# Kernel optimization log

Measured on AMD Instinct MI355X. Metric: run time of the kernel, lower is better.

The kernel has to match this reference:

```python
import jax, jax.numpy as jnp
import numpy as np

B, T, S = 1, 8, 1024
HID, H = 1152, 16
D = HID // H  # 72
EPS = 1e-6


def rmsnorm(t, gamma):
    # t: [b,t,s,h,d], gamma: [h,d] per-head learnable scale (QKNorm)
    var = jnp.mean(jnp.square(t), axis=-1, keepdims=True)
    return t * jax.lax.rsqrt(var + EPS) * gamma


def setup_inputs() -> dict:
    key = jax.random.key(0)
    ks = jax.random.split(key, 8)
    sc = lambda fan_in: 1.0 / np.sqrt(fan_in)
    x = jax.random.normal(ks[0], (B, T, S, HID), dtype=jnp.float32)
    Wq = jax.random.normal(ks[1], (HID, HID), dtype=jnp.float32) * sc(HID)
    bq = jnp.zeros((HID,), dtype=jnp.float32)
    Wkv = jax.random.normal(ks[2], (HID, 2 * HID), dtype=jnp.float32) * sc(HID)
    bkv = jnp.zeros((2 * HID,), dtype=jnp.float32)
    q_gamma = jnp.ones((H, D), dtype=jnp.float32)
    k_gamma = jnp.ones((H, D), dtype=jnp.float32)
    Wo = jax.random.normal(ks[3], (HID, HID), dtype=jnp.float32) * sc(HID)
    return {"x": x, "Wq": Wq, "bq": bq, "Wkv": Wkv, "bkv": bkv,
            "q_gamma": q_gamma, "k_gamma": k_gamma, "Wo": Wo}


def reference(x, Wq, bq, Wkv, bkv, q_gamma, k_gamma, Wo):
    b, t, s, _ = x.shape
    q = (x @ Wq + bq).reshape(b, t, s, H, D)
    kv = x @ Wkv + bkv
    k, v = jnp.split(kv, 2, axis=-1)
    k = k.reshape(b, t, s, H, D)
    v = v.reshape(b, t, s, H, D)
    q = rmsnorm(q, q_gamma)
    k = rmsnorm(k, k_gamma)
    # NOTE: original applies no 1/sqrt(d) scaling (QKNorm replaces it)
    attn_weight = jnp.einsum('btqhd,btkhd->bthqk', q, k)
    attn = jax.nn.softmax(attn_weight, axis=-1)
    out = jnp.einsum('bthqk,btkhd->btqhd', attn, v).reshape(b, t, s, HID)
    return out @ Wo
```

## Files before the change

kernel.cpp:

```cpp
#include <hip/hip_runtime.h>


typedef __attribute__((ext_vector_type(4))) short s16x4;
typedef __attribute__((ext_vector_type(8))) short s16x8;
typedef __attribute__((ext_vector_type(4))) float f32x4;
typedef __attribute__((ext_vector_type(16))) float f32x16;
typedef __attribute__((ext_vector_type(4))) int i32x4;

__device__ __forceinline__ unsigned short f2b(float x) {
  unsigned u = __float_as_uint(x);
  u += 0x7FFFu + ((u >> 16) & 1u);
  return (unsigned short)(u >> 16);
}
__device__ __forceinline__ float b2f(unsigned short u) {
  return __uint_as_float(((unsigned)u) << 16);
}
__device__ __forceinline__ void gld16(const void* g, void* l) {
  __builtin_amdgcn_global_load_lds(
      (const __attribute__((address_space(1))) void*)g,
      (__attribute__((address_space(3))) void*)l, 16, 0, 0);
}

__global__ __launch_bounds__(256) void cvt_bf16_kernel(const float* __restrict__ in,
                                                       unsigned short* __restrict__ out,
                                                       int n16) {
  int i = blockIdx.x * 256 + threadIdx.x;
  if (i >= n16) return;
  const float4* p = (const float4*)(in + (size_t)i * 16);
  float4 a = p[0], b = p[1], c = p[2], d = p[3];
  s16x8 r0, r1;
  r0[0] = (short)f2b(a.x); r0[1] = (short)f2b(a.y); r0[2] = (short)f2b(a.z); r0[3] = (short)f2b(a.w);
  r0[4] = (short)f2b(c.x); r0[5] = (short)f2b(c.y); r0[6] = (short)f2b(c.z); r0[7] = (short)f2b(c.w);
  r1[0] = (short)f2b(b.x); r1[1] = (short)f2b(b.y); r1[2] = (short)f2b(b.z); r1[3] = (short)f2b(b.w);
  r1[4] = (short)f2b(d.x); r1[5] = (short)f2b(d.y); r1[6] = (short)f2b(d.z); r1[7] = (short)f2b(d.w);
  *(s16x8*)(out + (size_t)i * 16) = r0;
  *(s16x8*)(out + (size_t)i * 16 + 8) = r1;
}

__global__ __launch_bounds__(256) void transpose_cvt3_kernel(
    const float* __restrict__ Wq, const float* __restrict__ Wkv,
    const float* __restrict__ Wo, unsigned short* __restrict__ WqT,
    unsigned short* __restrict__ WkvT, unsigned short* __restrict__ WoT) {
  constexpr int K = 1152;
  int id = blockIdx.x;
  const float* W;
  unsigned short* WT;
  int N;
  if (id < 1296) { W = Wq; WT = WqT; N = 1152; }
  else if (id < 3888) { W = Wkv; WT = WkvT; N = 2304; id -= 1296; }
  else { W = Wo; WT = WoT; N = 1152; id -= 3888; }
  int ntiles = N / 32;
  int bxx = id % ntiles, byy = id / ntiles;
  __shared__ float tile[32][33];
  int n0 = bxx * 32, k0 = byy * 32;
  int tx = threadIdx.x & 31, ty = threadIdx.x >> 5;
#pragma unroll
  for (int i = 0; i < 4; i++)
    tile[ty + i * 8][tx] = W[(size_t)(k0 + ty + i * 8) * N + n0 + tx];
  __syncthreads();
  int stx = (tx & 19) | ((tx & 4) << 1) | ((tx & 8) >> 1);
#pragma unroll
  for (int i = 0; i < 4; i++)
    WT[(size_t)(n0 + ty + i * 8) * K + k0 + stx] = f2b(tile[tx][ty + i * 8]);
}

__global__ __launch_bounds__(256) void gemm_qkv_kernel(const unsigned short* __restrict__ A,
                                                       const unsigned short* __restrict__ BT,
                                                       const float* __restrict__ biasq,
                                                       const float* __restrict__ biaskv,
                                                       unsigned short* __restrict__ qn,
                                                       unsigned short* __restrict__ kn,
                                                       unsigned short* __restrict__ vt) {
  constexpr int K = 1152;
  constexpr int NT = K / 32;
  __shared__ __align__(16) unsigned short LDSU[3 * 8192 + 3 * 4096];
  unsigned short* As = LDSU;
  unsigned short* Bs = LDSU + 3 * 8192;
  int tid = threadIdx.x;
  int lane = tid & 63, wave = tid >> 6;
  int wr = (wave >> 1) * 128, wc = (wave & 1) * 64;
  int l31 = lane & 31, lh = lane >> 5;
  int bid = blockIdx.x;
  int xcd = bid & 7;
  int w = bid >> 3;
  int st = w / 12, inner = w - st * 12;
  int ibx = inner % 3, iby = inner / 3;
  int bx = st * 3 + ibx;
  int by = xcd * 4 + iby;
  int brow = by * 256, bcol = bx * 128;
  const unsigned short* AsrcP[4];
  const unsigned short* BsrcP[2];
  int dstA[4], dstB[2];
#pragma unroll
  for (int i = 0; i < 4; i++) {
    int c = tid + 256 * i;
    int row = c >> 2, j = c & 3;
    AsrcP[i] = A + (size_t)(brow + row) * K + (j ^ ((row >> 1) & 3)) * 8;
    dstA[i] = (wave * 64 + 256 * i) * 8;
  }
#pragma unroll
  for (int i = 0; i < 2; i++) {
    int c = tid + 256 * i;
    int row = c >> 2, j = c & 3;
    BsrcP[i] = BT + (size_t)(bcol + row) * K + (j ^ ((row >> 1) & 3)) * 8;
    dstB[i] = (wave * 64 + 256 * i) * 8;
  }
#define STAGE(KT, BUF)                                           \
  {                                                              \
    int kb = (KT) * 32;                                          \
    gld16(AsrcP[0] + kb, &As[(BUF) * 8192 + dstA[0]]);           \
    gld16(AsrcP[1] + kb, &As[(BUF) * 8192 + dstA[1]]);           \
    gld16(AsrcP[2] + kb, &As[(BUF) * 8192 + dstA[2]]);           \
    gld16(AsrcP[3] + kb, &As[(BUF) * 8192 + dstA[3]]);           \
    gld16(BsrcP[0] + kb, &Bs[(BUF) * 4096 + dstB[0]]);           \
    gld16(BsrcP[1] + kb, &Bs[(BUF) * 4096 + dstB[1]]);           \
  }
  int fr = (l31 >> 1) & 3;
  int slotk[2] = {(lh ^ fr) * 8, ((2 + lh) ^ fr) * 8};
  STAGE(0, 0);
  STAGE(1, 1);
  f32x16 acc[4][2] = {};
  int cur = 0;
  for (int kt = 0; kt < NT; kt++) {
    if (kt < NT - 1)
      asm volatile("s_waitcnt vmcnt(6)\n\ts_barrier" ::: "memory");
    else
      asm volatile("s_waitcnt vmcnt(0)\n\ts_barrier" ::: "memory");
    if (kt + 2 < NT) {
      int nb = (cur == 0) ? 2 : cur - 1;
      STAGE(kt + 2, nb);
    }
    int ab = cur * 8192, bb = cur * 4096;
#pragma unroll
    for (int kk = 0; kk < 2; kk++) {
      int so = slotk[kk];
      s16x8 af[4], bf[2];
#pragma unroll
      for (int m = 0; m < 4; m++)
        af[m] = *(const s16x8*)&As[ab + (wr + m * 32 + l31) * 32 + so];
#pragma unroll
      for (int n = 0; n < 2; n++)
        bf[n] = *(const s16x8*)&Bs[bb + (wc + n * 32 + l31) * 32 + so];
      __builtin_amdgcn_s_setprio(1);
#pragma unroll
      for (int m = 0; m < 4; m++)
#pragma unroll
        for (int n = 0; n < 2; n++)
          acc[m][n] = __builtin_amdgcn_mfma_f32_32x32x16_bf16(af[m], bf[n], acc[m][n], 0, 0, 0);
      __builtin_amdgcn_s_setprio(0);
    }
    cur = (cur == 2) ? 0 : cur + 1;
  }
#undef STAGE
  if (bcol >= 2304) {
    __syncthreads();
    int c0 = bcol - 2304;
#pragma unroll
    for (int m = 0; m < 4; m++) {
#pragma unroll
      for (int n = 0; n < 2; n++) {
        int col = wc + n * 32 + l31;
        float bias = biaskv[1152 + c0 + col];
#pragma unroll
        for (int reg = 0; reg < 16; reg++) {
          int row = wr + m * 32 + (reg & 3) + 8 * (reg >> 2) + 4 * lh;
          LDSU[col * 264 + row] = f2b(acc[m][n][reg] + bias);
        }
      }
    }
    __syncthreads();
    int t = brow >> 10, sbase = brow & 1023;
#pragma unroll
    for (int i = 0; i < 16; i++) {
      int id = tid + 256 * i;
      int col = id >> 5, rowc = id & 31;
      int c = c0 + col;
      int h = c / 72, d = c - h * 72;
      s16x8 v8 = *(const s16x8*)&LDSU[col * 264 + rowc * 8];
      *(s16x8*)(vt + ((size_t)((t * 16 + h) * 80 + d)) * 1024 + sbase + rowc * 8) = v8;
    }
  } else {
#pragma unroll
    for (int m = 0; m < 4; m++) {
#pragma unroll
      for (int n = 0; n < 2; n++) {
        int gcol = bcol + wc + n * 32 + l31;
        float bias = (gcol < 1152) ? biasq[gcol] : biaskv[gcol - 1152];
        int c = (gcol < 1152) ? gcol : gcol - 1152;
        int h = c / 72, d = c - h * 72;
        unsigned short* dst = (gcol < 1152) ? qn : kn;
#pragma unroll
        for (int reg = 0; reg < 16; reg++) {
          int grow = brow + wr + m * 32 + (reg & 3) + 8 * (reg >> 2) + 4 * lh;
          float v = acc[m][n][reg] + bias;
          int t = grow >> 10, s = grow & 1023;
          dst[((size_t)((t * 16 + h) * 1024 + s)) * 96 + d] = f2b(v);
        }
      }
    }
  }
}

__global__ __launch_bounds__(256) void gemm_out_kernel(const unsigned short* __restrict__ A,
                                                       const unsigned short* __restrict__ BT,
                                                       int N, int gx,
                                                       float* __restrict__ outF) {
  constexpr int K = 1152;
  constexpr int NT = K / 32;
  __shared__ __align__(16) unsigned short As[3 * 4096];
  __shared__ __align__(16) unsigned short Bs[3 * 4096];
  int tid = threadIdx.x;
  int lane = tid & 63, wave = tid >> 6;
  int wr = (wave >> 1) * 64, wc = (wave & 1) * 64;
  int l31 = lane & 31, lh = lane >> 5;
  int bid = blockIdx.x;
  int xcd = bid & 7;
  int w = bid >> 3;
  int st = w / 24, inner = w - st * 24;
  int ibx = inner % 3, iby = inner / 3;
  int bx = st * 3 + ibx;
  int by = xcd * 8 + iby;
  int brow = by * 128, bcol = bx * 128;
  const unsigned short* AsrcP[2];
  const unsigned short* BsrcP[2];
  int dst0[2];
#pragma unroll
  for (int i = 0; i < 2; i++) {
    int c = tid + 256 * i;
    int row = c >> 2, j = c & 3;
    int ch = j ^ ((row >> 1) & 3);
    AsrcP[i] = A + (size_t)(brow + row) * K + ch * 8;
    BsrcP[i] = BT + (size_t)(bcol + row) * K + ch * 8;
    dst0[i] = (wave * 64 + 256 * i) * 8;
  }
#define STAGE(KT, BUF)                                          \
  {                                                             \
    int kb = (KT) * 32;                                         \
    gld16(AsrcP[0] + kb, &As[(BUF) * 4096 + dst0[0]]);          \
    gld16(BsrcP[0] + kb, &Bs[(BUF) * 4096 + dst0[0]]);          \
    gld16(AsrcP[1] + kb, &As[(BUF) * 4096 + dst0[1]]);          \
    gld16(BsrcP[1] + kb, &Bs[(BUF) * 4096 + dst0[1]]);          \
  }
  int fr = (l31 >> 1) & 3;
  int slotk[2] = {(lh ^ fr) * 8, ((2 + lh) ^ fr) * 8};
  STAGE(0, 0);
  STAGE(1, 1);
  f32x16 acc[2][2] = {};
  int cur = 0;
  for (int kt = 0; kt < NT; kt++) {
    if (kt < NT - 1)
      asm volatile("s_waitcnt vmcnt(4)\n\ts_barrier" ::: "memory");
    else
      asm volatile("s_waitcnt vmcnt(0)\n\ts_barrier" ::: "memory");
    if (kt + 2 < NT) {
      int nb = (cur == 0) ? 2 : cur - 1;
      STAGE(kt + 2, nb);
    }
    int ab = cur * 4096;
#pragma unroll
    for (int kk = 0; kk < 2; kk++) {
      int so = slotk[kk];
      s16x8 af[2], bf[2];
#pragma unroll
      for (int m = 0; m < 2; m++)
        af[m] = *(const s16x8*)&As[ab + (wr + m * 32 + l31) * 32 + so];
#pragma unroll
      for (int n = 0; n < 2; n++)
        bf[n] = *(const s16x8*)&Bs[ab + (wc + n * 32 + l31) * 32 + so];
      __builtin_amdgcn_s_setprio(1);
#pragma unroll
      for (int m = 0; m < 2; m++)
#pragma unroll
        for (int n = 0; n < 2; n++)
          acc[m][n] = __builtin_amdgcn_mfma_f32_32x32x16_bf16(af[m], bf[n], acc[m][n], 0, 0, 0);
      __builtin_amdgcn_s_setprio(0);
    }
    cur = (cur == 2) ? 0 : cur + 1;
  }
#undef STAGE
#pragma unroll
  for (int m = 0; m < 2; m++) {
#pragma unroll
    for (int n = 0; n < 2; n++) {
#pragma unroll
      for (int reg = 0; reg < 16; reg++) {
        int grow = brow + wr + m * 32 + (reg & 3) + 8 * (reg >> 2) + 4 * lh;
        int gcol = bcol + wc + n * 32 + l31;
        outF[(size_t)grow * N + gcol] = acc[m][n][reg];
      }
    }
  }
}

__global__ __launch_bounds__(256) void rmsnorm2_kernel(unsigned short* __restrict__ qn,
                                                       unsigned short* __restrict__ kn,
                                                       const float* __restrict__ qg,
                                                       const float* __restrict__ kg) {
  int r = blockIdx.x * 4 + (threadIdx.x >> 6);
  int isK = r >= 131072;
  int g = isK ? r - 131072 : r;
  unsigned short* buf = isK ? kn : qn;
  const float* gamma = isK ? kg : qg;
  int h = (g >> 10) & 15;
  size_t base = (size_t)g * 96;
  int l = threadIdx.x & 63;
  float e0 = b2f(buf[base + l]);
  float e1 = 0.f;
  if (l < 8) e1 = b2f(buf[base + 64 + l]);
  float ss = e0 * e0 + e1 * e1;
#pragma unroll
  for (int m = 1; m < 64; m <<= 1) ss += __shfl_xor(ss, m);
  float sc = rsqrtf(ss * (1.0f / 72.0f) + 1e-6f);
  buf[base + l] = f2b(e0 * sc * gamma[h * 72 + l]);
  if (l < 32) {
    float v = 0.f;
    if (l < 8) v = e1 * sc * gamma[h * 72 + 64 + l];
    buf[base + 64 + l] = f2b(v);
  }
}

__global__ __launch_bounds__(256) void attn_kernel(const unsigned short* __restrict__ Qn,
                                                   const unsigned short* __restrict__ Kn,
                                                   const unsigned short* __restrict__ VtG,
                                                   unsigned short* __restrict__ att) {
  __shared__ unsigned short Kl[2][64][100];
  __shared__ unsigned short Vt[80][76];
  int tid = threadIdx.x;
  int lane = tid & 63, wave = tid >> 6;
  int l15 = lane & 15, lq = lane >> 4, kf = lq * 4;
  int bid = blockIdx.x;
  int orig = (bid & 7) * 128 + (bid >> 3);
  int qb = orig & 7, th = orig >> 3;
  int t = th >> 4, h = th & 15;
  const unsigned short* Q = Qn + (size_t)th * 1024 * 96;
  const unsigned short* Kp = Kn + (size_t)th * 1024 * 96;
  const unsigned short* Vg = VtG + (size_t)th * 80 * 1024;
  int qrow0 = qb * 128 + wave * 32;
  int krow[3], kco[3], vd[3], vco[3];
#pragma unroll
  for (int i = 0; i < 3; i++) {
    int c = tid + i * 256;
    krow[i] = c / 12;
    kco[i] = c - 12 * krow[i];
    int cc = tid + i * 256;
    vd[i] = cc >> 3;
    vco[i] = cc & 7;
  }
  bool v2 = tid < 128;
  s16x8 sk[3], sv[3];
  s16x8 qf0[3], qf1[3];
#pragma unroll
  for (int c = 0; c < 3; c++) {
    const unsigned short* p0 = Q + (size_t)(qrow0 + l15) * 96 + c * 32 + kf;
    s16x4 lo = *(const s16x4*)p0;
    s16x4 hi = *(const s16x4*)(p0 + 16);
    qf0[c] = __builtin_shufflevector(lo, hi, 0, 1, 2, 3, 4, 5, 6, 7);
    const unsigned short* p1 = Q + (size_t)(qrow0 + 16 + l15) * 96 + c * 32 + kf;
    s16x4 lo1 = *(const s16x4*)p1;
    s16x4 hi1 = *(const s16x4*)(p1 + 16);
    qf1[c] = __builtin_shufflevector(lo1, hi1, 0, 1, 2, 3, 4, 5, 6, 7);
  }
  f32x4 o[2][5] = {};
  float m_r[2] = {-3.0e38f, -3.0e38f}, l_r[2] = {0.f, 0.f};

#pragma unroll
  for (int i = 0; i < 3; i++)
    sk[i] = *(const s16x8*)(Kp + (size_t)krow[i] * 96 + kco[i] * 8);
#pragma unroll
  for (int i = 0; i < 2; i++)
    sv[i] = *(const s16x8*)(Vg + (size_t)vd[i] * 1024 + vco[i] * 8);
  if (v2) sv[2] = *(const s16x8*)(Vg + (size_t)vd[2] * 1024 + vco[2] * 8);
#pragma unroll
  for (int i = 0; i < 3; i++) *(s16x8*)&Kl[0][krow[i]][kco[i] * 8] = sk[i];
#pragma unroll
  for (int i = 0; i < 2; i++) *(s16x8*)&Vt[vd[i]][vco[i] * 8] = sv[i];
  if (v2) *(s16x8*)&Vt[vd[2]][vco[2] * 8] = sv[2];

  for (int tt = 0; tt < 16; tt++) {
    __syncthreads();
    int cur = tt & 1;
    if (tt < 15) {
      int kv1 = (tt + 1) * 64;
#pragma unroll
      for (int i = 0; i < 3; i++)
        sk[i] = *(const s16x8*)(Kp + (size_t)(kv1 + krow[i]) * 96 + kco[i] * 8);
#pragma unroll
      for (int i = 0; i < 2; i++)
        sv[i] = *(const s16x8*)(Vg + (size_t)vd[i] * 1024 + kv1 + vco[i] * 8);
      if (v2) sv[2] = *(const s16x8*)(Vg + (size_t)vd[2] * 1024 + kv1 + vco[2] * 8);
    }
    f32x4 st0[4], st1[4];
    __builtin_amdgcn_s_setprio(1);
#pragma unroll
    for (int n = 0; n < 4; n++) {
      f32x4 a0 = {}, a1 = {};
#pragma unroll
      for (int c = 0; c < 3; c++) {
        s16x4 lo = *(const s16x4*)&Kl[cur][n * 16 + l15][c * 32 + kf];
        s16x4 hi = *(const s16x4*)&Kl[cur][n * 16 + l15][c * 32 + kf + 16];
        s16x8 kfr = __builtin_shufflevector(lo, hi, 0, 1, 2, 3, 4, 5, 6, 7);
        a0 = __builtin_amdgcn_mfma_f32_16x16x32_bf16(kfr, qf0[c], a0, 0, 0, 0);
        a1 = __builtin_amdgcn_mfma_f32_16x16x32_bf16(kfr, qf1[c], a1, 0, 0, 0);
      }
      st0[n] = a0;
      st1[n] = a1;
    }
    __builtin_amdgcn_s_setprio(0);
#define SOFTMAX(ST, G)                                                        \
    {                                                                         \
      float tmax = ST[0][0];                                                  \
      _Pragma("unroll") for (int n = 0; n < 4; n++)                           \
        _Pragma("unroll") for (int r = 0; r < 4; r++)                         \
          tmax = fmaxf(tmax, ST[n][r]);                                       \
      tmax = fmaxf(tmax, __shfl_xor(tmax, 16));                               \
      tmax = fmaxf(tmax, __shfl_xor(tmax, 32));                               \
      bool up = !__all(tmax <= m_r[G]);                                       \
      float scale = 1.0f;                                                     \
      if (up) {                                                               \
        float mn = fmaxf(m_r[G], tmax);                                       \
        scale = __expf(m_r[G] - mn);                                          \
        m_r[G] = mn;                                                          \
      }                                                                       \
      float sum = 0.f;                                                        \
      _Pragma("unroll") for (int n = 0; n < 4; n++)                           \
        _Pragma("unroll") for (int r = 0; r < 4; r++) {                       \
          float p = __expf(ST[n][r] - m_r[G]);                                \
          ST[n][r] = p;                                                       \
          sum += p;                                                           \
        }                                                                     \
      sum += __shfl_xor(sum, 16);                                             \
      sum += __shfl_xor(sum, 32);                                             \
      if (up) {                                                               \
        l_r[G] = l_r[G] * scale + sum;                                        \
        _Pragma("unroll") for (int r = 0; r < 4; r++) {                       \
          float scq = __shfl(scale, 4 * lq + r);                              \
          _Pragma("unroll") for (int v = 0; v < 5; v++) o[G][v][r] *= scq;    \
        }                                                                     \
      } else {                                                                \
        l_r[G] += sum;                                                        \
      }                                                                       \
    }
#define PV(ST, G)                                                             \
    {                                                                         \
      __builtin_amdgcn_s_setprio(1);                                          \
      _Pragma("unroll") for (int b = 0; b < 2; b++) {                         \
        int w0, w1, w2, w3;                                                   \
        asm("v_cvt_pk_bf16_f32 %0, %1, %2" : "=v"(w0)                         \
            : "v"(ST[2 * b][0]), "v"(ST[2 * b][1]));                          \
        asm("v_cvt_pk_bf16_f32 %0, %1, %2" : "=v"(w1)                         \
            : "v"(ST[2 * b][2]), "v"(ST[2 * b][3]));                          \
        asm("v_cvt_pk_bf16_f32 %0, %1, %2" : "=v"(w2)                         \
            : "v"(ST[2 * b + 1][0]), "v"(ST[2 * b + 1][1]));                  \
        asm("v_cvt_pk_bf16_f32 %0, %1, %2" : "=v"(w3)                         \
            : "v"(ST[2 * b + 1][2]), "v"(ST[2 * b + 1][3]));                  \
        i32x4 pw = {w0, w1, w2, w3};                                          \
        s16x8 pf = __builtin_bit_cast(s16x8, pw);                             \
        _Pragma("unroll") for (int v = 0; v < 5; v++) {                       \
          s16x4 vlo = *(const s16x4*)&Vt[v * 16 + l15][b * 32 + kf];          \
          s16x4 vhi = *(const s16x4*)&Vt[v * 16 + l15][b * 32 + kf + 16];     \
          s16x8 vf = __builtin_shufflevector(vlo, vhi, 0, 1, 2, 3, 4, 5, 6, 7);\
          o[G][v] = __builtin_amdgcn_mfma_f32_16x16x32_bf16(pf, vf, o[G][v], 0, 0, 0); \
        }                                                                     \
      }                                                                       \
      __builtin_amdgcn_s_setprio(0);                                          \
    }
    SOFTMAX(st0, 0);
    PV(st0, 0);
    SOFTMAX(st1, 1);
    PV(st1, 1);
#undef SOFTMAX
#undef PV
    if (tt < 15) {
      __syncthreads();
      int nxt = cur ^ 1;
#pragma unroll
      for (int i = 0; i < 3; i++) *(s16x8*)&Kl[nxt][krow[i]][kco[i] * 8] = sk[i];
#pragma unroll
      for (int i = 0; i < 2; i++) *(s16x8*)&Vt[vd[i]][vco[i] * 8] = sv[i];
      if (v2) *(s16x8*)&Vt[vd[2]][vco[2] * 8] = sv[2];
    }
  }
#pragma unroll
  for (int g = 0; g < 2; g++)
#pragma unroll
    for (int r = 0; r < 4; r++) {
      float inv = 1.0f / __shfl(l_r[g], 4 * lq + r);
      int qrow = qrow0 + g * 16 + 4 * lq + r;
      size_t rowbase = (size_t)(t * 1024 + qrow) * 1152;
#pragma unroll
      for (int v = 0; v < 5; v++) {
        int d = v * 16 + l15;
        if (d < 72) {
          int col = h * 72 + d;
          int scol = (col & ~12) | ((col & 4) << 1) | ((col & 8) >> 1);
          att[rowbase + scol] = f2b(o[g][v][r] * inv);
        }
      }
    }
}

extern "C" void kernel_launch(void* const* d_in, const int* in_sizes, int n_in,
                              void* d_out, int out_size, void* d_ws, size_t ws_size,
                              hipStream_t stream) {
  const float* x   = (const float*)d_in[0];
  const float* Wq  = (const float*)d_in[1];
  const float* bq  = (const float*)d_in[2];
  const float* Wkv = (const float*)d_in[3];
  const float* bkv = (const float*)d_in[4];
  const float* qg  = (const float*)d_in[5];
  const float* kg  = (const float*)d_in[6];
  const float* Wo  = (const float*)d_in[7];
  float* out = (float*)d_out;

  char* w = (char*)d_ws;
  unsigned short* xb   = (unsigned short*)w; w += (size_t)8192 * 1152 * 2;
  unsigned short* WqT  = (unsigned short*)w; w += (size_t)1152 * 1152 * 2;
  unsigned short* WkvT = (unsigned short*)w; w += (size_t)2304 * 1152 * 2;
  unsigned short* WoT  = (unsigned short*)w; w += (size_t)1152 * 1152 * 2;
  unsigned short* qn   = (unsigned short*)w; w += (size_t)128 * 1024 * 96 * 2;
  unsigned short* kn   = (unsigned short*)w; w += (size_t)128 * 1024 * 96 * 2;
  unsigned short* vt   = (unsigned short*)w; w += (size_t)128 * 80 * 1024 * 2;
  unsigned short* att  = (unsigned short*)w; w += (size_t)8192 * 1152 * 2;

  cvt_bf16_kernel<<<2304, 256, 0, stream>>>(x, xb, 9437184 / 16);
  transpose_cvt3_kernel<<<5184, 256, 0, stream>>>(Wq, Wkv, Wo, WqT, WkvT, WoT);

  gemm_qkv_kernel<<<864, 256, 0, stream>>>(xb, WqT, bq, bkv, qn, kn, vt);
  rmsnorm2_kernel<<<65536, 256, 0, stream>>>(qn, kn, qg, kg);

  attn_kernel<<<1024, 256, 0, stream>>>(qn, kn, vt, att);

  gemm_out_kernel<<<576, 256, 0, stream>>>(att, WoT, 1152, 9, out);
}
```

Before: 302.4 us.

## Enlarge output GEMM tile to 256x128 and share V fragments across query groups

The output projection GEMM now uses 256x128 block tiles, with each wave computing 128x64. This halves the grid to 288 blocks and re-maps block indices per XCD. It raises data reuse per loaded tile, at the cost of more LDS and accumulator registers and fewer blocks than the 256 CUs. In the attention kernel, PV for both query groups now runs after both softmaxes and shares each V fragment load between two MFMAs, which cuts LDS reads but keeps both probability tiles live longer.

```diff
diff --git a/kernel.cpp b/kernel.cpp
--- a/kernel.cpp
+++ b/kernel.cpp
@@ -203,73 +203,77 @@
 
 __global__ __launch_bounds__(256) void gemm_out_kernel(const unsigned short* __restrict__ A,
                                                        const unsigned short* __restrict__ BT,
-                                                       int N, int gx,
                                                        float* __restrict__ outF) {
   constexpr int K = 1152;
   constexpr int NT = K / 32;
-  __shared__ __align__(16) unsigned short As[3 * 4096];
+  __shared__ __align__(16) unsigned short As[3 * 8192];
   __shared__ __align__(16) unsigned short Bs[3 * 4096];
   int tid = threadIdx.x;
   int lane = tid & 63, wave = tid >> 6;
-  int wr = (wave >> 1) * 64, wc = (wave & 1) * 64;
+  int wr = (wave >> 1) * 128, wc = (wave & 1) * 64;
   int l31 = lane & 31, lh = lane >> 5;
   int bid = blockIdx.x;
   int xcd = bid & 7;
   int w = bid >> 3;
-  int st = w / 24, inner = w - st * 24;
-  int ibx = inner % 3, iby = inner / 3;
-  int bx = st * 3 + ibx;
-  int by = xcd * 8 + iby;
-  int brow = by * 128, bcol = bx * 128;
-  const unsigned short* AsrcP[2];
+  int iby = w / 9, bx = w - iby * 9;
+  int by = xcd * 4 + iby;
+  int brow = by * 256, bcol = bx * 128;
+  const unsigned short* AsrcP[4];
   const unsigned short* BsrcP[2];
-  int dst0[2];
+  int dstA[4], dstB[2];
+#pragma unroll
+  for (int i = 0; i < 4; i++) {
+    int c = tid + 256 * i;
+    int row = c >> 2, j = c & 3;
+    AsrcP[i] = A + (size_t)(brow + row) * K + (j ^ ((row >> 1) & 3)) * 8;
+    dstA[i] = (wave * 64 + 256 * i) * 8;
+  }
 #pragma unroll
   for (int i = 0; i < 2; i++) {
     int c = tid + 256 * i;
     int row = c >> 2, j = c & 3;
-    int ch = j ^ ((row >> 1) & 3);
-    AsrcP[i] = A + (size_t)(brow + row) * K + ch * 8;
-    BsrcP[i] = BT + (size_t)(bcol + row) * K + ch * 8;
-    dst0[i] = (wave * 64 + 256 * i) * 8;
-  }
-#define STAGE(KT, BUF)                                          \
-  {                                                             \
-    int kb = (KT) * 32;                                         \
-    gld16(AsrcP[0] + kb, &As[(BUF) * 4096 + dst0[0]]);          \
-    gld16(BsrcP[0] + kb, &Bs[(BUF) * 4096 + dst0[0]]);          \
-    gld16(AsrcP[1] + kb, &As[(BUF) * 4096 + dst0[1]]);          \
-    gld16(BsrcP[1] + kb, &Bs[(BUF) * 4096 + dst0[1]]);          \
+    BsrcP[i] = BT + (size_t)(bcol + row) * K + (j ^ ((row >> 1) & 3)) * 8;
+    dstB[i] = (wave * 64 + 256 * i) * 8;
+  }
+#define STAGE(KT, BUF)                                           \
+  {                                                              \
+    int kb = (KT) * 32;                                          \
+    gld16(AsrcP[0] + kb, &As[(BUF) * 8192 + dstA[0]]);           \
+    gld16(AsrcP[1] + kb, &As[(BUF) * 8192 + dstA[1]]);           \
+    gld16(AsrcP[2] + kb, &As[(BUF) * 8192 + dstA[2]]);           \
+    gld16(AsrcP[3] + kb, &As[(BUF) * 8192 + dstA[3]]);           \
+    gld16(BsrcP[0] + kb, &Bs[(BUF) * 4096 + dstB[0]]);           \
+    gld16(BsrcP[1] + kb, &Bs[(BUF) * 4096 + dstB[1]]);           \
   }
   int fr = (l31 >> 1) & 3;
   int slotk[2] = {(lh ^ fr) * 8, ((2 + lh) ^ fr) * 8};
   STAGE(0, 0);
   STAGE(1, 1);
-  f32x16 acc[2][2] = {};
+  f32x16 acc[4][2] = {};
   int cur = 0;
   for (int kt = 0; kt < NT; kt++) {
     if (kt < NT - 1)
-      asm volatile("s_waitcnt vmcnt(4)\n\ts_barrier" ::: "memory");
+      asm volatile("s_waitcnt vmcnt(6)\n\ts_barrier" ::: "memory");
     else
       asm volatile("s_waitcnt vmcnt(0)\n\ts_barrier" ::: "memory");
     if (kt + 2 < NT) {
       int nb = (cur == 0) ? 2 : cur - 1;
       STAGE(kt + 2, nb);
     }
-    int ab = cur * 4096;
+    int ab = cur * 8192, bb = cur * 4096;
 #pragma unroll
     for (int kk = 0; kk < 2; kk++) {
       int so = slotk[kk];
-      s16x8 af[2], bf[2];
-#pragma unroll
-      for (int m = 0; m < 2; m++)
+      s16x8 af[4], bf[2];
+#pragma unroll
+      for (int m = 0; m < 4; m++)
         af[m] = *(const s16x8*)&As[ab + (wr + m * 32 + l31) * 32 + so];
 #pragma unroll
       for (int n = 0; n < 2; n++)
-        bf[n] = *(const s16x8*)&Bs[ab + (wc + n * 32 + l31) * 32 + so];
+        bf[n] = *(const s16x8*)&Bs[bb + (wc + n * 32 + l31) * 32 + so];
       __builtin_amdgcn_s_setprio(1);
 #pragma unroll
-      for (int m = 0; m < 2; m++)
+      for (int m = 0; m < 4; m++)
 #pragma unroll
         for (int n = 0; n < 2; n++)
           acc[m][n] = __builtin_amdgcn_mfma_f32_32x32x16_bf16(af[m], bf[n], acc[m][n], 0, 0, 0);
@@ -279,14 +283,14 @@
   }
 #undef STAGE
 #pragma unroll
-  for (int m = 0; m < 2; m++) {
+  for (int m = 0; m < 4; m++) {
 #pragma unroll
     for (int n = 0; n < 2; n++) {
 #pragma unroll
       for (int reg = 0; reg < 16; reg++) {
         int grow = brow + wr + m * 32 + (reg & 3) + 8 * (reg >> 2) + 4 * lh;
         int gcol = bcol + wc + n * 32 + l31;
-        outF[(size_t)grow * N + gcol] = acc[m][n][reg];
+        outF[(size_t)grow * 1152 + gcol] = acc[m][n][reg];
       }
     }
   }
@@ -440,36 +444,35 @@
         l_r[G] += sum;                                                        \
       }                                                                       \
     }
-#define PV(ST, G)                                                             \
-    {                                                                         \
-      __builtin_amdgcn_s_setprio(1);                                          \
-      _Pragma("unroll") for (int b = 0; b < 2; b++) {                         \
-        int w0, w1, w2, w3;                                                   \
-        asm("v_cvt_pk_bf16_f32 %0, %1, %2" : "=v"(w0)                         \
-            : "v"(ST[2 * b][0]), "v"(ST[2 * b][1]));                          \
-        asm("v_cvt_pk_bf16_f32 %0, %1, %2" : "=v"(w1)                         \
-            : "v"(ST[2 * b][2]), "v"(ST[2 * b][3]));                          \
-        asm("v_cvt_pk_bf16_f32 %0, %1, %2" : "=v"(w2)                         \
-            : "v"(ST[2 * b + 1][0]), "v"(ST[2 * b + 1][1]));                  \
-        asm("v_cvt_pk_bf16_f32 %0, %1, %2" : "=v"(w3)                         \
-            : "v"(ST[2 * b + 1][2]), "v"(ST[2 * b + 1][3]));                  \
-        i32x4 pw = {w0, w1, w2, w3};                                          \
-        s16x8 pf = __builtin_bit_cast(s16x8, pw);                             \
-        _Pragma("unroll") for (int v = 0; v < 5; v++) {                       \
-          s16x4 vlo = *(const s16x4*)&Vt[v * 16 + l15][b * 32 + kf];          \
-          s16x4 vhi = *(const s16x4*)&Vt[v * 16 + l15][b * 32 + kf + 16];     \
-          s16x8 vf = __builtin_shufflevector(vlo, vhi, 0, 1, 2, 3, 4, 5, 6, 7);\
-          o[G][v] = __builtin_amdgcn_mfma_f32_16x16x32_bf16(pf, vf, o[G][v], 0, 0, 0); \
-        }                                                                     \
-      }                                                                       \
-      __builtin_amdgcn_s_setprio(0);                                          \
-    }
     SOFTMAX(st0, 0);
-    PV(st0, 0);
     SOFTMAX(st1, 1);
-    PV(st1, 1);
 #undef SOFTMAX
-#undef PV
+    __builtin_amdgcn_s_setprio(1);
+#pragma unroll
+    for (int b = 0; b < 2; b++) {
+      int a0, a1, a2, a3, b0w, b1w, b2w, b3w;
+      asm("v_cvt_pk_bf16_f32 %0, %1, %2" : "=v"(a0) : "v"(st0[2 * b][0]), "v"(st0[2 * b][1]));
+      asm("v_cvt_pk_bf16_f32 %0, %1, %2" : "=v"(a1) : "v"(st0[2 * b][2]), "v"(st0[2 * b][3]));
+      asm("v_cvt_pk_bf16_f32 %0, %1, %2" : "=v"(a2) : "v"(st0[2 * b + 1][0]), "v"(st0[2 * b + 1][1]));
+      asm("v_cvt_pk_bf16_f32 %0, %1, %2" : "=v"(a3) : "v"(st0[2 * b + 1][2]), "v"(st0[2 * b + 1][3]));
+      asm("v_cvt_pk_bf16_f32 %0, %1, %2" : "=v"(b0w) : "v"(st1[2 * b][0]), "v"(st1[2 * b][1]));
+      asm("v_cvt_pk_bf16_f32 %0, %1, %2" : "=v"(b1w) : "v"(st1[2 * b][2]), "v"(st1[2 * b][3]));
+      asm("v_cvt_pk_bf16_f32 %0, %1, %2" : "=v"(b2w) : "v"(st1[2 * b + 1][0]), "v"(st1[2 * b + 1][1]));
+      asm("v_cvt_pk_bf16_f32 %0, %1, %2" : "=v"(b3w) : "v"(st1[2 * b + 1][2]), "v"(st1[2 * b + 1][3]));
+      i32x4 pw0 = {a0, a1, a2, a3};
+      i32x4 pw1 = {b0w, b1w, b2w, b3w};
+      s16x8 pf0 = __builtin_bit_cast(s16x8, pw0);
+      s16x8 pf1 = __builtin_bit_cast(s16x8, pw1);
+#pragma unroll
+      for (int v = 0; v < 5; v++) {
+        s16x4 vlo = *(const s16x4*)&Vt[v * 16 + l15][b * 32 + kf];
+        s16x4 vhi = *(const s16x4*)&Vt[v * 16 + l15][b * 32 + kf + 16];
+        s16x8 vf = __builtin_shufflevector(vlo, vhi, 0, 1, 2, 3, 4, 5, 6, 7);
+        o[0][v] = __builtin_amdgcn_mfma_f32_16x16x32_bf16(pf0, vf, o[0][v], 0, 0, 0);
+        o[1][v] = __builtin_amdgcn_mfma_f32_16x16x32_bf16(pf1, vf, o[1][v], 0, 0, 0);
+      }
+    }
+    __builtin_amdgcn_s_setprio(0);
     if (tt < 15) {
       __syncthreads();
       int nxt = cur ^ 1;
@@ -530,5 +533,5 @@
 
   attn_kernel<<<1024, 256, 0, stream>>>(qn, kn, vt, att);
 
-  gemm_out_kernel<<<576, 256, 0, stream>>>(att, WoT, 1152, 9, out);
-}
+  gemm_out_kernel<<<288, 256, 0, stream>>>(att, WoT, out);
+}
```

Measured after the change: 299.3 us. No clear change (-1.0%).
